# Kernel optimization log

Hardware: AMD Instinct MI355X
Metric: run time of the kernel (lower is better)

## Reference

```python
import jax, jax.numpy as jnp
import numpy as np

K = 1024
H = 16
HEAD = K // H

def setup_inputs() -> dict:
    key = jax.random.key(0)
    ks = jax.random.split(key, 6)
    b, t = 2, 2048
    x = jax.random.normal(ks[0], (b, t, K), dtype=jnp.float32)
    padding = jnp.ones((b, t), dtype=jnp.int32)
    s = 1.0 / np.sqrt(K)
    Wq = jax.random.normal(ks[1], (K, K), dtype=jnp.float32) * s
    Wk = jax.random.normal(ks[2], (K, K), dtype=jnp.float32) * s
    Wv = jax.random.normal(ks[3], (K, K), dtype=jnp.float32) * s
    Wo = jax.random.normal(ks[4], (K, K), dtype=jnp.float32) * s
    bo = jnp.zeros((K,), dtype=jnp.float32)
    return {"x": x, "padding": padding, "Wq": Wq, "Wk": Wk, "Wv": Wv, "Wo": Wo, "bo": bo}

def reference(x, padding, Wq, Wk, Wv, Wo, bo):
    b, t, k = x.shape
    h, d = H, HEAD
    # projections (nn.Linear: x @ W.T), then split heads -> [b,h,t,d]
    q = (x @ Wq.T).reshape(b, t, h, d).transpose(0, 2, 1, 3)
    kk = (x @ Wk.T).reshape(b, t, h, d).transpose(0, 2, 1, 3)
    v = (x @ Wv.T).reshape(b, t, h, d).transpose(0, 2, 1, 3)
    scores = jnp.einsum('bhqd,bhkd->bhqk', q, kk)
    # key-side padding mask: positions with padding==0 get -inf (before scaling,
    # same result since -inf/sqrt(d) == -inf)
    mask = (padding == 0)[:, None, None, :]  # [b,1,1,t]
    scores = jnp.where(mask, -jnp.inf, scores) / np.sqrt(d).astype(np.float32)
    weights = jax.nn.softmax(scores, axis=-1)
    out = jnp.einsum('bhqk,bhkd->bhqd', weights, v)
    out = out.transpose(0, 2, 1, 3).reshape(b, t, h * d)
    return out @ Wo.T + bo
```

## Files before the change

### kernel.cpp

```cpp
#include <hip/hip_runtime.h>
#include <hip/hip_bf16.h>
#include <cmath>
#include <stdint.h>

#define K_DIM 1024
#define NH    16
#define HD    64
#define T     2048
#define NTOK  4096
#define NBH   32

typedef __bf16 bf16x8 __attribute__((ext_vector_type(8)));
typedef float  f32x4  __attribute__((ext_vector_type(4)));
typedef short  s16x4  __attribute__((ext_vector_type(4)));

__device__ __forceinline__ unsigned short f2bf(float f) {
  union { float f; unsigned u; } v; v.f = f;
  unsigned u = v.u;
  return (unsigned short)((u + 0x7FFFu + ((u >> 16) & 1u)) >> 16);
}
__device__ __forceinline__ ushort4 pk4(float a, float b, float c, float d) {
  union { __hip_bfloat162 h[2]; ushort4 u; } r;
  r.h[0] = __float22bfloat162_rn(float2{a, b});
  r.h[1] = __float22bfloat162_rn(float2{c, d});
  return r.u;
}
__device__ __forceinline__ int pk2(float a, float b) {
  union { __hip_bfloat162 h; int u; } r;
  r.h = __float22bfloat162_rn(float2{a, b});
  return r.u;
}

__device__ __forceinline__ void gload16(const void* g, void* l) {
  __builtin_amdgcn_global_load_lds(
      (__attribute__((address_space(1))) void*)(g),
      (__attribute__((address_space(3))) void*)(l),
      16, 0, 0);
}

__global__ void convert_kernel(const float* __restrict__ x,
                               const float* __restrict__ Wq,
                               const float* __restrict__ Wk,
                               const float* __restrict__ Wv,
                               const float* __restrict__ Wo,
                               unsigned short* __restrict__ xb,
                               unsigned short* __restrict__ wqkv,
                               unsigned short* __restrict__ wob)
{
  const size_t NX = (size_t)NTOK * K_DIM;
  const size_t NW = (size_t)K_DIM * K_DIM;
  size_t i = ((size_t)blockIdx.x * blockDim.x + threadIdx.x) * 4;
  const float* src; unsigned short* dst; size_t off;
  float scale = 1.f;
  if (i < NX)             { src = x;  dst = xb;          off = i; }
  else if (i < NX + NW)   { src = Wq; dst = wqkv;        off = i - NX;
                            scale = 0.18033688011112042f; }
  else if (i < NX + 2*NW) { src = Wk; dst = wqkv + NW;   off = i - NX - NW; }
  else if (i < NX + 3*NW) { src = Wv; dst = wqkv + 2*NW; off = i - NX - 2*NW; }
  else                    { src = Wo; dst = wob;         off = i - NX - 3*NW; }
  float4 v = *(const float4*)(src + off);
  *(ushort4*)(dst + off) = pk4(v.x * scale, v.y * scale, v.z * scale, v.w * scale);
}

template <int MODE, int TM, int TN>
__global__ __launch_bounds__(256, 2)
void gemm_bt(const unsigned short* __restrict__ A,
             const unsigned short* __restrict__ B,
             unsigned short* __restrict__ o_q,
             unsigned short* __restrict__ o_k,
             unsigned short* __restrict__ o_v,
             float* __restrict__ o_f,
             const float* __restrict__ bias)
{
  __shared__ unsigned short Asm[TM * 64];
  __shared__ unsigned short Bsm[TN * 64];
  const int tid  = threadIdx.x;
  const int wave = tid >> 6;
  const int lane = tid & 63;
  const int lq   = lane & 15;
  const int quad = lane >> 4;
  const int bm = blockIdx.x, bn = blockIdx.y;
  const int wm = (wave >> 1) * (TM / 2), wn = (wave & 1) * (TN / 2);
  const int MT = TM / 32, NT = TN / 32;

  f32x4 acc[MT][NT];
#pragma unroll
  for (int i = 0; i < MT; ++i)
#pragma unroll
    for (int j = 0; j < NT; ++j) acc[i][j] = (f32x4){0.f, 0.f, 0.f, 0.f};

  const char* Ab = (const char*)(A + (size_t)bm * TM * K_DIM);
  const char* Bb = (const char*)(B + (size_t)bn * TN * K_DIM);

  for (int k0 = 0; k0 < K_DIM; k0 += 64) {
#pragma unroll
    for (int i = 0; i < MT; ++i) {
      int off   = i * 4096 + wave * 1024 + lane * 16;
      int row   = off >> 7;
      int chunk = (off >> 4) & 7;
      int scol  = (chunk ^ (row & 7)) << 4;
      gload16(Ab + (size_t)row * (K_DIM * 2) + (size_t)k0 * 2 + scol,
              (char*)Asm + off - lane * 16);
    }
#pragma unroll
    for (int i = 0; i < NT; ++i) {
      int off   = i * 4096 + wave * 1024 + lane * 16;
      int row   = off >> 7;
      int chunk = (off >> 4) & 7;
      int scol  = (chunk ^ (row & 7)) << 4;
      gload16(Bb + (size_t)row * (K_DIM * 2) + (size_t)k0 * 2 + scol,
              (char*)Bsm + off - lane * 16);
    }
    __syncthreads();
#pragma unroll
    for (int kk = 0; kk < 64; kk += 32) {
      bf16x8 af[MT], bfr[NT];
#pragma unroll
      for (int mt = 0; mt < MT; ++mt) {
        int row = wm + mt * 16 + lq;
        int sw  = (quad + (kk >> 3)) ^ (row & 7);
        af[mt] = *(const bf16x8*)((const char*)Asm + row * 128 + (sw << 4));
      }
#pragma unroll
      for (int nt = 0; nt < NT; ++nt) {
        int row = wn + nt * 16 + lq;
        int sw  = (quad + (kk >> 3)) ^ (row & 7);
        bfr[nt] = *(const bf16x8*)((const char*)Bsm + row * 128 + (sw << 4));
      }
#pragma unroll
      for (int mt = 0; mt < MT; ++mt)
#pragma unroll
        for (int nt = 0; nt < NT; ++nt)
          acc[mt][nt] = __builtin_amdgcn_mfma_f32_16x16x32_bf16(af[mt], bfr[nt], acc[mt][nt], 0, 0, 0);
    }
    __syncthreads();
  }

#pragma unroll
  for (int mt = 0; mt < MT; ++mt) {
    int mbase = bm * TM + wm + mt * 16 + quad * 4;
#pragma unroll
    for (int nt = 0; nt < NT; ++nt) {
      int n = bn * TN + wn + nt * 16 + lq;
      if (MODE == 1) {
        int which = mbase >> 10, c = mbase & 1023;
        int h = c >> 6, d0 = c & 63;
        int b = n >> 11, t = n & 2047;
        if (which < 2) {
          ushort4 pk = pk4(acc[mt][nt][0], acc[mt][nt][1], acc[mt][nt][2], acc[mt][nt][3]);
          unsigned short* dst = which ? o_k : o_q;
          *(ushort4*)&dst[((size_t)(b * NH + h) * T + t) * HD + d0] = pk;
        } else {
#pragma unroll
          for (int r = 0; r < 4; ++r)
            o_v[((size_t)(b * NH + h) * HD + d0 + r) * T + t] = f2bf(acc[mt][nt][r]);
        }
      } else {
        float4 bv = *(const float4*)&bias[mbase];
        float4 o;
        o.x = acc[mt][nt][0] + bv.x; o.y = acc[mt][nt][1] + bv.y;
        o.z = acc[mt][nt][2] + bv.z; o.w = acc[mt][nt][3] + bv.w;
        *(float4*)&o_f[(size_t)n * K_DIM + mbase] = o;
      }
    }
  }
}

__global__ __launch_bounds__(256, 2)
void attn_kernel(const unsigned short* __restrict__ Q,
                 const unsigned short* __restrict__ Kb,
                 const unsigned short* __restrict__ Vt,
                 const int* __restrict__ padding,
                 unsigned short* __restrict__ O)
{
  __shared__ unsigned short Ksm[128 * 64];
  __shared__ unsigned short Vsm[2][64 * 128];

  const int tid  = threadIdx.x;
  const int wave = tid >> 6;
  const int lane = tid & 63;
  const int lq   = lane & 15;
  const int quad = lane >> 4;
  const int bh = blockIdx.x;
  const int qt = blockIdx.y;
  const int b  = bh >> 4;
  const int h  = bh & 15;
  const int qbase = qt * 128 + wave * 32;

  bf16x8 qf[2][2];
#pragma unroll
  for (int nq = 0; nq < 2; ++nq)
#pragma unroll
    for (int kk = 0; kk < 2; ++kk)
      qf[nq][kk] = *(const bf16x8*)&Q[((size_t)bh * T + qbase + nq * 16 + lq) * HD + kk * 32 + quad * 8];

  f32x4 o_acc[2][4];
#pragma unroll
  for (int nq = 0; nq < 2; ++nq)
#pragma unroll
    for (int nd = 0; nd < 4; ++nd) o_acc[nq][nd] = (f32x4){0.f, 0.f, 0.f, 0.f};
  float l_part[2] = {0.f, 0.f};

  auto stage = [&](int kt, int buf) {
#pragma unroll
    for (int i = 0; i < 4; ++i) {
      int off = i * 4096 + wave * 1024 + lane * 16;
      {
        int row = off >> 7, chunk = (off >> 4) & 7;
        int scol = (chunk ^ (row & 7)) << 4;
        gload16((const char*)Kb + ((size_t)(bh * T + kt * 128 + row) * HD) * 2 + scol,
                (char*)Ksm + off - lane * 16);
      }
      {
        int row = off >> 8, chunk = (off >> 4) & 15;
        int scol = (chunk ^ (row & 15)) << 4;
        gload16((const char*)Vt + ((size_t)(bh * HD + row) * T + (size_t)kt * 128) * 2 + scol,
                (char*)Vsm[buf] + off - lane * 16);
      }
    }
  };

  stage(0, 0);
  __syncthreads();

  for (int kt = 0; kt < T / 128; ++kt) {
    const int cur = kt & 1;

    f32x4 st[8][2];
#pragma unroll
    for (int nt = 0; nt < 8; ++nt)
#pragma unroll
      for (int nq = 0; nq < 2; ++nq) st[nt][nq] = (f32x4){0.f, 0.f, 0.f, 0.f};
#pragma unroll
    for (int kk = 0; kk < 2; ++kk) {
#pragma unroll
      for (int nt = 0; nt < 8; ++nt) {
        int row = nt * 16 + lq;
        int sw  = (quad + kk * 4) ^ (row & 7);
        bf16x8 kf = *(const bf16x8*)((const char*)Ksm + row * 128 + (sw << 4));
        st[nt][0] = __builtin_amdgcn_mfma_f32_16x16x32_bf16(kf, qf[0][kk], st[nt][0], 0, 0, 0);
        st[nt][1] = __builtin_amdgcn_mfma_f32_16x16x32_bf16(kf, qf[1][kk], st[nt][1], 0, 0, 0);
      }
    }

    __syncthreads();

    if (kt < T / 128 - 1) stage(kt + 1, cur ^ 1);

    union PA { int d[2]; s16x4 v; } pa[8][2];
#pragma unroll
    for (int nt = 0; nt < 8; ++nt) {
      int4 pd = *(const int4*)&padding[b * T + kt * 128 + nt * 16 + quad * 4];
#pragma unroll
      for (int nq = 0; nq < 2; ++nq) {
        float p0 = pd.x ? __builtin_amdgcn_exp2f(st[nt][nq][0]) : 0.f;
        float p1 = pd.y ? __builtin_amdgcn_exp2f(st[nt][nq][1]) : 0.f;
        float p2 = pd.z ? __builtin_amdgcn_exp2f(st[nt][nq][2]) : 0.f;
        float p3 = pd.w ? __builtin_amdgcn_exp2f(st[nt][nq][3]) : 0.f;
        l_part[nq] += (p0 + p1) + (p2 + p3);
        pa[nt][nq].d[0] = pk2(p0, p1);
        pa[nt][nq].d[1] = pk2(p2, p3);
      }
    }

#pragma unroll
    for (int nt = 0; nt < 8; ++nt) {
#pragma unroll
      for (int nd = 0; nd < 4; ++nd) {
        int row = nd * 16 + lq;
        int g   = 2 * nt + (quad >> 1);
        int sw  = g ^ (row & 15);
        s16x4 vf = *(const s16x4*)((const char*)Vsm[cur] + row * 256 + (sw << 4) + ((quad & 1) << 3));
        o_acc[0][nd] = __builtin_amdgcn_mfma_f32_16x16x16bf16_1k(pa[nt][0].v, vf, o_acc[0][nd], 0, 0, 0);
        o_acc[1][nd] = __builtin_amdgcn_mfma_f32_16x16x16bf16_1k(pa[nt][1].v, vf, o_acc[1][nd], 0, 0, 0);
      }
    }

    __syncthreads();
  }

  float linv[2];
#pragma unroll
  for (int nq = 0; nq < 2; ++nq) {
    float lsum = l_part[nq];
    lsum += __shfl_xor(lsum, 16);
    lsum += __shfl_xor(lsum, 32);
    linv[nq] = (lsum > 0.f) ? 1.f / lsum : 0.f;
  }
#pragma unroll
  for (int nq = 0; nq < 2; ++nq) {
#pragma unroll
    for (int r = 0; r < 4; ++r) {
      float iv = __shfl(linv[nq], quad * 4 + r);
      int t = qbase + nq * 16 + quad * 4 + r;
#pragma unroll
      for (int nd = 0; nd < 4; ++nd) {
        int chan = h * HD + nd * 16 + lq;
        O[((size_t)(b * T + t)) * K_DIM + chan] = f2bf(o_acc[nq][nd][r] * iv);
      }
    }
  }
}

extern "C" void kernel_launch(void* const* d_in, const int* in_sizes, int n_in,
                              void* d_out, int out_size, void* d_ws, size_t ws_size,
                              hipStream_t stream)
{
  const float* x       = (const float*)d_in[0];
  const int*   padding = (const int*)d_in[1];
  const float* Wq      = (const float*)d_in[2];
  const float* Wk      = (const float*)d_in[3];
  const float* Wv      = (const float*)d_in[4];
  const float* Wo      = (const float*)d_in[5];
  const float* bo      = (const float*)d_in[6];
  float* out = (float*)d_out;

  char* ws = (char*)d_ws;
  unsigned short* xb   = (unsigned short*)(ws);
  unsigned short* wqkv = (unsigned short*)(ws + (8u  << 20));
  unsigned short* wob  = (unsigned short*)(ws + (14u << 20));
  unsigned short* qb   = (unsigned short*)(ws + (16u << 20));
  unsigned short* kb   = (unsigned short*)(ws + (24u << 20));
  unsigned short* vtb  = (unsigned short*)(ws + (32u << 20));
  unsigned short* ab   = (unsigned short*)(ws + (40u << 20));

  convert_kernel<<<8192, 256, 0, stream>>>(x, Wq, Wk, Wv, Wo, xb, wqkv, wob);

  gemm_bt<1, 192, 128><<<dim3(16, 32), 256, 0, stream>>>(wqkv, xb, qb, kb, vtb, nullptr, nullptr);

  attn_kernel<<<dim3(32, 16), 256, 0, stream>>>(qb, kb, vtb, padding, ab);

  gemm_bt<2, 64, 128><<<dim3(16, 32), 256, 0, stream>>>(wob, ab, nullptr, nullptr, nullptr, out, bo);
}
```

Baseline: 188.7 us.

## Switch attention kernel to 32x32x16 bf16 MFMA with permlane32 swaps for P layout

```diff
diff --git a/kernel.cpp b/kernel.cpp
--- a/kernel.cpp
+++ b/kernel.cpp
@@ -12,7 +12,7 @@
 
 typedef __bf16 bf16x8 __attribute__((ext_vector_type(8)));
 typedef float  f32x4  __attribute__((ext_vector_type(4)));
-typedef short  s16x4  __attribute__((ext_vector_type(4)));
+typedef float  f32x16 __attribute__((ext_vector_type(16)));
 
 __device__ __forceinline__ unsigned short f2bf(float f) {
   union { float f; unsigned u; } v; v.f = f;
@@ -175,31 +175,30 @@
 {
   __shared__ unsigned short Ksm[128 * 64];
   __shared__ unsigned short Vsm[2][64 * 128];
+  __shared__ float Lsm[4][32];
 
   const int tid  = threadIdx.x;
   const int wave = tid >> 6;
   const int lane = tid & 63;
-  const int lq   = lane & 15;
-  const int quad = lane >> 4;
+  const int l31  = lane & 31;
+  const int hw   = lane >> 5;
   const int bh = blockIdx.x;
   const int qt = blockIdx.y;
   const int b  = bh >> 4;
   const int h  = bh & 15;
   const int qbase = qt * 128 + wave * 32;
 
-  bf16x8 qf[2][2];
-#pragma unroll
-  for (int nq = 0; nq < 2; ++nq)
-#pragma unroll
-    for (int kk = 0; kk < 2; ++kk)
-      qf[nq][kk] = *(const bf16x8*)&Q[((size_t)bh * T + qbase + nq * 16 + lq) * HD + kk * 32 + quad * 8];
-
-  f32x4 o_acc[2][4];
-#pragma unroll
-  for (int nq = 0; nq < 2; ++nq)
-#pragma unroll
-    for (int nd = 0; nd < 4; ++nd) o_acc[nq][nd] = (f32x4){0.f, 0.f, 0.f, 0.f};
-  float l_part[2] = {0.f, 0.f};
+  bf16x8 qf[4];
+#pragma unroll
+  for (int kk = 0; kk < 4; ++kk)
+    qf[kk] = *(const bf16x8*)&Q[((size_t)bh * T + qbase + l31) * HD + kk * 16 + hw * 8];
+
+  f32x16 o_acc[2];
+#pragma unroll
+  for (int db = 0; db < 2; ++db)
+#pragma unroll
+    for (int r = 0; r < 16; ++r) o_acc[db][r] = 0.f;
+  float l_part = 0.f;
 
   auto stage = [&](int kt, int buf) {
 #pragma unroll
@@ -226,20 +225,19 @@
   for (int kt = 0; kt < T / 128; ++kt) {
     const int cur = kt & 1;
 
-    f32x4 st[8][2];
-#pragma unroll
-    for (int nt = 0; nt < 8; ++nt)
-#pragma unroll
-      for (int nq = 0; nq < 2; ++nq) st[nt][nq] = (f32x4){0.f, 0.f, 0.f, 0.f};
-#pragma unroll
-    for (int kk = 0; kk < 2; ++kk) {
-#pragma unroll
-      for (int nt = 0; nt < 8; ++nt) {
-        int row = nt * 16 + lq;
-        int sw  = (quad + kk * 4) ^ (row & 7);
+    f32x16 st[4];
+#pragma unroll
+    for (int nt = 0; nt < 4; ++nt)
+#pragma unroll
+      for (int r = 0; r < 16; ++r) st[nt][r] = 0.f;
+#pragma unroll
+    for (int kk = 0; kk < 4; ++kk) {
+#pragma unroll
+      for (int nt = 0; nt < 4; ++nt) {
+        int row = nt * 32 + l31;
+        int sw  = (2 * kk + hw) ^ (row & 7);
         bf16x8 kf = *(const bf16x8*)((const char*)Ksm + row * 128 + (sw << 4));
-        st[nt][0] = __builtin_amdgcn_mfma_f32_16x16x32_bf16(kf, qf[0][kk], st[nt][0], 0, 0, 0);
-        st[nt][1] = __builtin_amdgcn_mfma_f32_16x16x32_bf16(kf, qf[1][kk], st[nt][1], 0, 0, 0);
+        st[nt] = __builtin_amdgcn_mfma_f32_32x32x16_bf16(kf, qf[kk], st[nt], 0, 0, 0);
       }
     }
 
@@ -247,57 +245,66 @@
 
     if (kt < T / 128 - 1) stage(kt + 1, cur ^ 1);
 
-    union PA { int d[2]; s16x4 v; } pa[8][2];
-#pragma unroll
-    for (int nt = 0; nt < 8; ++nt) {
-      int4 pd = *(const int4*)&padding[b * T + kt * 128 + nt * 16 + quad * 4];
-#pragma unroll
-      for (int nq = 0; nq < 2; ++nq) {
-        float p0 = pd.x ? __builtin_amdgcn_exp2f(st[nt][nq][0]) : 0.f;
-        float p1 = pd.y ? __builtin_amdgcn_exp2f(st[nt][nq][1]) : 0.f;
-        float p2 = pd.z ? __builtin_amdgcn_exp2f(st[nt][nq][2]) : 0.f;
-        float p3 = pd.w ? __builtin_amdgcn_exp2f(st[nt][nq][3]) : 0.f;
-        l_part[nq] += (p0 + p1) + (p2 + p3);
-        pa[nt][nq].d[0] = pk2(p0, p1);
-        pa[nt][nq].d[1] = pk2(p2, p3);
-      }
-    }
-
-#pragma unroll
-    for (int nt = 0; nt < 8; ++nt) {
-#pragma unroll
-      for (int nd = 0; nd < 4; ++nd) {
-        int row = nd * 16 + lq;
-        int g   = 2 * nt + (quad >> 1);
-        int sw  = g ^ (row & 15);
-        s16x4 vf = *(const s16x4*)((const char*)Vsm[cur] + row * 256 + (sw << 4) + ((quad & 1) << 3));
-        o_acc[0][nd] = __builtin_amdgcn_mfma_f32_16x16x16bf16_1k(pa[nt][0].v, vf, o_acc[0][nd], 0, 0, 0);
-        o_acc[1][nd] = __builtin_amdgcn_mfma_f32_16x16x16bf16_1k(pa[nt][1].v, vf, o_acc[1][nd], 0, 0, 0);
+#pragma unroll
+    for (int nt = 0; nt < 4; ++nt) {
+      int dw[8];
+#pragma unroll
+      for (int g = 0; g < 4; ++g) {
+        int4 pd = *(const int4*)&padding[b * T + kt * 128 + nt * 32 + g * 8 + hw * 4];
+        float p0 = pd.x ? __builtin_amdgcn_exp2f(st[nt][g * 4 + 0]) : 0.f;
+        float p1 = pd.y ? __builtin_amdgcn_exp2f(st[nt][g * 4 + 1]) : 0.f;
+        float p2 = pd.z ? __builtin_amdgcn_exp2f(st[nt][g * 4 + 2]) : 0.f;
+        float p3 = pd.w ? __builtin_amdgcn_exp2f(st[nt][g * 4 + 3]) : 0.f;
+        l_part += (p0 + p1) + (p2 + p3);
+        dw[g * 2]     = pk2(p0, p1);
+        dw[g * 2 + 1] = pk2(p2, p3);
+      }
+      union PA { int d[4]; bf16x8 v; } pa0, pa1;
+      {
+        int a0 = dw[0], c0 = dw[2];
+        int a1 = dw[1], c1 = dw[3];
+        asm("v_permlane32_swap_b32 %0, %1" : "+v"(a0), "+v"(c0));
+        asm("v_permlane32_swap_b32 %0, %1" : "+v"(a1), "+v"(c1));
+        pa0.d[0] = a0; pa0.d[1] = a1; pa0.d[2] = c0; pa0.d[3] = c1;
+        int b0 = dw[4], d0 = dw[6];
+        int b1 = dw[5], d1 = dw[7];
+        asm("v_permlane32_swap_b32 %0, %1" : "+v"(b0), "+v"(d0));
+        asm("v_permlane32_swap_b32 %0, %1" : "+v"(b1), "+v"(d1));
+        pa1.d[0] = b0; pa1.d[1] = b1; pa1.d[2] = d0; pa1.d[3] = d1;
+      }
+#pragma unroll
+      for (int j = 0; j < 2; ++j) {
+        bf16x8 pav = j ? pa1.v : pa0.v;
+#pragma unroll
+        for (int db = 0; db < 2; ++db) {
+          int row = db * 32 + l31;
+          int g2  = 4 * nt + 2 * j + hw;
+          int sw  = g2 ^ (row & 15);
+          bf16x8 vf = *(const bf16x8*)((const char*)Vsm[cur] + row * 256 + (sw << 4));
+          o_acc[db] = __builtin_amdgcn_mfma_f32_32x32x16_bf16(pav, vf, o_acc[db], 0, 0, 0);
+        }
       }
     }
 
     __syncthreads();
   }
 
-  float linv[2];
-#pragma unroll
-  for (int nq = 0; nq < 2; ++nq) {
-    float lsum = l_part[nq];
-    lsum += __shfl_xor(lsum, 16);
-    lsum += __shfl_xor(lsum, 32);
-    linv[nq] = (lsum > 0.f) ? 1.f / lsum : 0.f;
-  }
-#pragma unroll
-  for (int nq = 0; nq < 2; ++nq) {
-#pragma unroll
-    for (int r = 0; r < 4; ++r) {
-      float iv = __shfl(linv[nq], quad * 4 + r);
-      int t = qbase + nq * 16 + quad * 4 + r;
-#pragma unroll
-      for (int nd = 0; nd < 4; ++nd) {
-        int chan = h * HD + nd * 16 + lq;
-        O[((size_t)(b * T + t)) * K_DIM + chan] = f2bf(o_acc[nq][nd][r] * iv);
-      }
+  float lsum = l_part + __shfl_xor(l_part, 32);
+  float inv  = (lsum > 0.f) ? 1.f / lsum : 0.f;
+  Lsm[wave][l31] = inv;
+  __syncthreads();
+  f32x4 inv4[4];
+#pragma unroll
+  for (int g = 0; g < 4; ++g)
+    inv4[g] = *(const f32x4*)&Lsm[wave][g * 8 + hw * 4];
+#pragma unroll
+  for (int db = 0; db < 2; ++db) {
+#pragma unroll
+    for (int r = 0; r < 16; ++r) {
+      int qrow = (r & 3) + 8 * (r >> 2) + 4 * hw;
+      int t    = qbase + qrow;
+      int chan = h * HD + db * 32 + l31;
+      O[((size_t)(b * T + t)) * K_DIM + chan] = f2bf(o_acc[db][r] * inv4[r >> 2][r & 3]);
     }
   }
 }
```

Result: slower. 205.0 us (+8.6%).
